# Performance work log

Measured on AMD Instinct MI355X. Metric: run time of the kernel, lower is better.

## Reference

```python
import jax, jax.numpy as jnp
import numpy as np

D_MODEL = 256; N_LAYERS = 4; INPUT_LEN = 15
D_INNER = 512; D_STATE = 16; D_CONV = 4; DT_RANK = 16
BATCH = 4; SEQ = 2048; EPS = 1e-5

def _ln(x, w, b):
    m = jnp.mean(x, -1, keepdims=True)
    v = jnp.var(x, -1, keepdims=True)
    return (x - m) * jax.lax.rsqrt(v + EPS) * w + b

def _silu(x):
    return x * jax.nn.sigmoid(x)

def _mixer(h, inW, cw, cb, xpW, dtW, dtb, A_log, Dp, opW):
    # h: [B,L,d_model]
    xz = h @ inW.T                      # [B,L,2*D_INNER]
    xh, z = jnp.split(xz, 2, axis=-1)
    # causal depthwise conv1d
    xc = jnp.transpose(xh, (0, 2, 1))   # [B,D,L]
    xc = jax.lax.conv_general_dilated(xc, cw, (1,), [(D_CONV - 1, 0)],
                                      feature_group_count=D_INNER,
                                      dimension_numbers=('NCH', 'OIH', 'NCH'))
    xc = xc + cb[None, :, None]
    xh = _silu(jnp.transpose(xc, (0, 2, 1)))  # [B,L,D]
    dbl = xh @ xpW.T                    # [B,L,DT_RANK+2N]
    dt = dbl[..., :DT_RANK]
    Bm = dbl[..., DT_RANK:DT_RANK + D_STATE]
    C = dbl[..., DT_RANK + D_STATE:]
    dt = jax.nn.softplus(dt @ dtW.T + dtb)    # [B,L,D]
    A = -jnp.exp(A_log)                       # [D,N]
    dA = jnp.exp(dt[..., None] * A)           # [B,L,D,N]
    dBu = dt[..., None] * Bm[:, :, None, :] * xh[..., None]  # [B,L,D,N]
    def step(hst, inp):
        dA_t, dBu_t, C_t = inp
        hst = dA_t * hst + dBu_t
        y = jnp.einsum('bdn,bn->bd', hst, C_t)
        return hst, y
    h0 = jnp.zeros((xh.shape[0], D_INNER, D_STATE), xh.dtype)
    _, ys = jax.lax.scan(step, h0, (jnp.transpose(dA, (1, 0, 2, 3)),
                                    jnp.transpose(dBu, (1, 0, 2, 3)),
                                    jnp.transpose(C, (1, 0, 2))))
    y = jnp.transpose(ys, (1, 0, 2)) + Dp * xh
    y = y * _silu(z)
    return y @ opW.T

def setup_inputs():
    key = jax.random.key(0)
    ks = jax.random.split(key, 8)
    s = 0.02
    return {
        'x_src': jax.random.normal(ks[0], (BATCH, SEQ, INPUT_LEN), jnp.float32),
        'single_eval_pos': 1024,
        'in_W': jax.random.normal(ks[1], (D_MODEL, INPUT_LEN)) * s,
        'norm_w': jnp.ones((N_LAYERS, D_MODEL)),
        'norm_b': jnp.zeros((N_LAYERS, D_MODEL)),
        'inproj_W': jax.random.normal(ks[2], (N_LAYERS, 2 * D_INNER, D_MODEL)) * s,
        'conv_w': jax.random.normal(ks[3], (N_LAYERS, D_INNER, 1, D_CONV)) * 0.2,
        'conv_b': jnp.zeros((N_LAYERS, D_INNER)),
        'xproj_W': jax.random.normal(ks[4], (N_LAYERS, DT_RANK + 2 * D_STATE, D_INNER)) * s,
        'dtproj_W': jax.random.normal(ks[5], (N_LAYERS, D_INNER, DT_RANK)) * 0.1,
        'dtproj_b': jnp.log(jnp.expm1(jnp.full((N_LAYERS, D_INNER), 0.01))),
        'A_log': jnp.log(jnp.broadcast_to(jnp.arange(1, D_STATE + 1, dtype=jnp.float32), (N_LAYERS, D_INNER, D_STATE)) + 0.0),
        'D_param': jnp.ones((N_LAYERS, D_INNER)),
        'outproj_W': jax.random.normal(ks[6], (N_LAYERS, D_MODEL, D_INNER)) * s,
        'out_W': jax.random.normal(ks[7], (1, D_MODEL)) * s,
    }

def reference(x_src, single_eval_pos, in_W, norm_w, norm_b, inproj_W, conv_w, conv_b, xproj_W, dtproj_W, dtproj_b, A_log, D_param, outproj_W, out_W):
    h = x_src @ in_W.T                  # [B,L,d_model]
    res = None
    for i in range(N_LAYERS):
        res = h if res is None else h + res
        hn = _ln(res, norm_w[i], norm_b[i])
        h = _mixer(hn, inproj_W[i], conv_w[i], conv_b[i], xproj_W[i],
                   dtproj_W[i], dtproj_b[i], A_log[i], D_param[i], outproj_W[i])
    # backbone returns hidden_states directly (norm_f defined but not applied)
    return h @ out_W.T                  # [B,L,1]
```

## Files before the change

kernel.cpp:

```cpp
#include <hip/hip_runtime.h>

#define B_   4
#define T_   2048
#define BT_  8192
#define INL  15
#define DM   256
#define DI   512
#define DX   1024
#define DS_  16
#define DR_  16
#define NO_  48
#define NL   4
#define NC_  128
#define LCH  16

typedef short bf16x8 __attribute__((ext_vector_type(8)));
typedef float f32x4  __attribute__((ext_vector_type(4)));

__device__ __forceinline__ float sigmoidf_(float x){ return 1.f/(1.f+__expf(-x)); }

__device__ __forceinline__ unsigned short f2bf(float x){
    union { float f; unsigned u; } v; v.f = x;
    unsigned r = (v.u + 0x7FFFu + ((v.u >> 16) & 1u)) >> 16;
    return (unsigned short)r;
}
__device__ __forceinline__ float bf2f(unsigned short h){
    union { unsigned u; float f; } v; v.u = ((unsigned)h) << 16;
    return v.f;
}

__device__ __forceinline__ void ld16(const float* __restrict__ p, float* v){
    const float4* q = (const float4*)p;
    float4 x0=q[0],x1=q[1],x2=q[2],x3=q[3];
    v[0]=x0.x; v[1]=x0.y; v[2]=x0.z; v[3]=x0.w;
    v[4]=x1.x; v[5]=x1.y; v[6]=x1.z; v[7]=x1.w;
    v[8]=x2.x; v[9]=x2.y; v[10]=x2.z; v[11]=x2.w;
    v[12]=x3.x; v[13]=x3.y; v[14]=x3.z; v[15]=x3.w;
}
__device__ __forceinline__ void st16(float* __restrict__ p, const float* v){
    float4* q = (float4*)p;
    q[0] = make_float4(v[0],v[1],v[2],v[3]);
    q[1] = make_float4(v[4],v[5],v[6],v[7]);
    q[2] = make_float4(v[8],v[9],v[10],v[11]);
    q[3] = make_float4(v[12],v[13],v[14],v[15]);
}

__global__ void k_cvtW3(const float* __restrict__ W0, unsigned short* __restrict__ h0,
                        unsigned short* __restrict__ l0, int n0,
                        const float* __restrict__ W1, unsigned short* __restrict__ h1,
                        unsigned short* __restrict__ l1, int n1,
                        const float* __restrict__ W2, unsigned short* __restrict__ h2,
                        unsigned short* __restrict__ l2, int n2){
    int g = blockIdx.x*256 + threadIdx.x;
    const float* W; unsigned short *hi, *lo; int idx;
    if(g < n0){ W = W0; hi = h0; lo = l0; idx = g; }
    else if(g < n0+n1){ W = W1; hi = h1; lo = l1; idx = g - n0; }
    else if(g < n0+n1+n2){ W = W2; hi = h2; lo = l2; idx = g - n0 - n1; }
    else return;
    float4 v = ((const float4*)W)[idx];
    ushort4 h, l;
    h.x = f2bf(v.x); l.x = f2bf(v.x - bf2f(h.x));
    h.y = f2bf(v.y); l.y = f2bf(v.y - bf2f(h.y));
    h.z = f2bf(v.z); l.z = f2bf(v.z - bf2f(h.z));
    h.w = f2bf(v.w); l.w = f2bf(v.w - bf2f(h.w));
    ((ushort4*)hi)[idx] = h;
    ((ushort4*)lo)[idx] = l;
}

__global__ void k_inln(const float* __restrict__ x, const float* __restrict__ W,
                       float* __restrict__ res,
                       unsigned short* __restrict__ hnhi, unsigned short* __restrict__ hnlo,
                       const float* __restrict__ w, const float* __restrict__ b){
    int wv = threadIdx.x >> 6, lane = threadIdx.x & 63;
    int bt = blockIdx.x*4 + wv;
    const float* xr = x + bt*INL;
    float xl[INL];
#pragma unroll
    for(int k=0;k<INL;k++) xl[k] = xr[k];
    float4 v;
    float* vv = (float*)&v;
#pragma unroll
    for(int j=0;j<4;j++){
        int m = lane*4 + j;
        const float* wr = W + m*INL;
        float acc = 0.f;
#pragma unroll
        for(int k=0;k<INL;k++) acc += xl[k]*wr[k];
        vv[j] = acc;
    }
    ((float4*)(res + (size_t)bt*DM))[lane] = v;
    float s  = v.x+v.y+v.z+v.w;
    float ss = v.x*v.x+v.y*v.y+v.z*v.z+v.w*v.w;
#pragma unroll
    for(int m=1;m<64;m<<=1){ s += __shfl_xor(s,m); ss += __shfl_xor(ss,m); }
    float mean = s*(1.f/DM);
    float var  = ss*(1.f/DM) - mean*mean;
    float inv  = rsqrtf(var + 1e-5f);
    float4 wt = ((const float4*)w)[lane];
    float4 bs = ((const float4*)b)[lane];
    float4 o;
    o.x = (v.x-mean)*inv*wt.x + bs.x;
    o.y = (v.y-mean)*inv*wt.y + bs.y;
    o.z = (v.z-mean)*inv*wt.z + bs.z;
    o.w = (v.w-mean)*inv*wt.w + bs.w;
    ushort4 hh, ll;
    hh.x = f2bf(o.x); ll.x = f2bf(o.x - bf2f(hh.x));
    hh.y = f2bf(o.y); ll.y = f2bf(o.y - bf2f(hh.y));
    hh.z = f2bf(o.z); ll.z = f2bf(o.z - bf2f(hh.z));
    hh.w = f2bf(o.w); ll.w = f2bf(o.w - bf2f(hh.w));
    ((ushort4*)(hnhi + (size_t)bt*DM))[lane] = hh;
    ((ushort4*)(hnlo + (size_t)bt*DM))[lane] = ll;
}

__global__ void k_resln(const float* __restrict__ h, float* __restrict__ res,
                        unsigned short* __restrict__ hnhi, unsigned short* __restrict__ hnlo,
                        const float* __restrict__ w, const float* __restrict__ b, int addRes){
    int wv = threadIdx.x >> 6, lane = threadIdx.x & 63;
    int bt = blockIdx.x*4 + wv;
    float4 v = ((const float4*)(h + (size_t)bt*DM))[lane];
    if(addRes){
        float4 r = ((const float4*)(res + (size_t)bt*DM))[lane];
        v.x+=r.x; v.y+=r.y; v.z+=r.z; v.w+=r.w;
    }
    ((float4*)(res + (size_t)bt*DM))[lane] = v;
    float s  = v.x+v.y+v.z+v.w;
    float ss = v.x*v.x+v.y*v.y+v.z*v.z+v.w*v.w;
#pragma unroll
    for(int m=1;m<64;m<<=1){ s += __shfl_xor(s,m); ss += __shfl_xor(ss,m); }
    float mean = s*(1.f/DM);
    float var  = ss*(1.f/DM) - mean*mean;
    float inv  = rsqrtf(var + 1e-5f);
    float4 wt = ((const float4*)w)[lane];
    float4 bs = ((const float4*)b)[lane];
    float4 o;
    o.x = (v.x-mean)*inv*wt.x + bs.x;
    o.y = (v.y-mean)*inv*wt.y + bs.y;
    o.z = (v.z-mean)*inv*wt.z + bs.z;
    o.w = (v.w-mean)*inv*wt.w + bs.w;
    ushort4 hh, ll;
    hh.x = f2bf(o.x); ll.x = f2bf(o.x - bf2f(hh.x));
    hh.y = f2bf(o.y); ll.y = f2bf(o.y - bf2f(hh.y));
    hh.z = f2bf(o.z); ll.z = f2bf(o.z - bf2f(hh.z));
    hh.w = f2bf(o.w); ll.w = f2bf(o.w - bf2f(hh.w));
    ((ushort4*)(hnhi + (size_t)bt*DM))[lane] = hh;
    ((ushort4*)(hnlo + (size_t)bt*DM))[lane] = ll;
}

template<int BM,int BN>
__global__ void __launch_bounds__(256) k_gemm_bf3(
    const unsigned short* __restrict__ Ahi, const unsigned short* __restrict__ Alo,
    const unsigned short* __restrict__ Bhi, const unsigned short* __restrict__ Blo,
    float* __restrict__ C, int M, int N, int K)
{
    constexpr int LDP = 40;
    constexpr int WM = BM/2, WN = BN/2;
    constexpr int MI_ = WM/16, NI_ = WN/16;
    __shared__ unsigned short sAh[BM*LDP], sAl[BM*LDP], sBh[BN*LDP], sBl[BN*LDP];
    int tid  = threadIdx.x;
    int wave = tid >> 6, lane = tid & 63;
    int wm0  = (wave >> 1) * WM, wn0 = (wave & 1) * WN;
    int m0   = blockIdx.y * BM, n0 = blockIdx.x * BN;
    int lr   = lane & 15;
    int kq   = (lane >> 4) * 8;
    int quad4 = (lane >> 4) * 4;

    f32x4 acc[MI_][NI_];
#pragma unroll
    for(int i=0;i<MI_;i++)
#pragma unroll
        for(int j=0;j<NI_;j++) acc[i][j] = (f32x4){0.f,0.f,0.f,0.f};

    for(int k0=0;k0<K;k0+=32){
#pragma unroll
        for(int i=tid;i<BM*4;i+=256){
            int r = i>>2, cg = (i&3)*8;
            size_t go = (size_t)(m0+r)*K + k0 + cg;
            *(float4*)(&sAh[r*LDP + cg]) = *(const float4*)(Ahi + go);
            *(float4*)(&sAl[r*LDP + cg]) = *(const float4*)(Alo + go);
        }
#pragma unroll
        for(int i=tid;i<BN*4;i+=256){
            int r = i>>2, cg = (i&3)*8;
            size_t go = (size_t)(n0+r)*K + k0 + cg;
            *(float4*)(&sBh[r*LDP + cg]) = *(const float4*)(Bhi + go);
            *(float4*)(&sBl[r*LDP + cg]) = *(const float4*)(Blo + go);
        }
        __syncthreads();
        bf16x8 ah[MI_], al[MI_], bh[NI_], bl[NI_];
#pragma unroll
        for(int mi=0;mi<MI_;mi++){
            int ro = (wm0 + mi*16 + lr)*LDP + kq;
            ah[mi] = *(const bf16x8*)(&sAh[ro]);
            al[mi] = *(const bf16x8*)(&sAl[ro]);
        }
#pragma unroll
        for(int ni=0;ni<NI_;ni++){
            int ro = (wn0 + ni*16 + lr)*LDP + kq;
            bh[ni] = *(const bf16x8*)(&sBh[ro]);
            bl[ni] = *(const bf16x8*)(&sBl[ro]);
        }
#pragma unroll
        for(int mi=0;mi<MI_;mi++)
#pragma unroll
            for(int ni=0;ni<NI_;ni++){
                acc[mi][ni] = __builtin_amdgcn_mfma_f32_16x16x32_bf16(ah[mi], bh[ni], acc[mi][ni], 0,0,0);
                acc[mi][ni] = __builtin_amdgcn_mfma_f32_16x16x32_bf16(ah[mi], bl[ni], acc[mi][ni], 0,0,0);
                acc[mi][ni] = __builtin_amdgcn_mfma_f32_16x16x32_bf16(al[mi], bh[ni], acc[mi][ni], 0,0,0);
            }
        __syncthreads();
    }
#pragma unroll
    for(int mi=0;mi<MI_;mi++)
#pragma unroll
        for(int ni=0;ni<NI_;ni++){
            int col = n0 + wn0 + ni*16 + lr;
#pragma unroll
            for(int r=0;r<4;r++){
                int row = m0 + wm0 + mi*16 + quad4 + r;
                C[(size_t)row*N + col] = acc[mi][ni][r];
            }
        }
}

template<int BM,int BN>
__global__ void __launch_bounds__(256) k_gemm_pk(
    const unsigned* __restrict__ Apk,
    const unsigned short* __restrict__ Bhi, const unsigned short* __restrict__ Blo,
    float* __restrict__ C, int M, int N, int K)
{
    constexpr int LDP = 40;
    constexpr int WM = BM/2, WN = BN/2;
    constexpr int MI_ = WM/16, NI_ = WN/16;
    __shared__ unsigned short sAh[BM*LDP], sAl[BM*LDP], sBh[BN*LDP], sBl[BN*LDP];
    int tid  = threadIdx.x;
    int wave = tid >> 6, lane = tid & 63;
    int wm0  = (wave >> 1) * WM, wn0 = (wave & 1) * WN;
    int m0   = blockIdx.y * BM, n0 = blockIdx.x * BN;
    int lr   = lane & 15;
    int kq   = (lane >> 4) * 8;
    int quad4 = (lane >> 4) * 4;

    f32x4 acc[MI_][NI_];
#pragma unroll
    for(int i=0;i<MI_;i++)
#pragma unroll
        for(int j=0;j<NI_;j++) acc[i][j] = (f32x4){0.f,0.f,0.f,0.f};

    for(int k0=0;k0<K;k0+=32){
#pragma unroll
        for(int i=tid;i<BM*2;i+=256){
            int r = i>>1, hf = (i&1)*16;
            const uint4* yp = (const uint4*)(Apk + (size_t)(m0+r)*K + k0 + hf);
#pragma unroll
            for(int q=0;q<4;q++){
                uint4 p = yp[q];
                ushort4 H, L;
                H.x=(unsigned short)p.x;  L.x=(unsigned short)(p.x>>16);
                H.y=(unsigned short)p.y;  L.y=(unsigned short)(p.y>>16);
                H.z=(unsigned short)p.z;  L.z=(unsigned short)(p.z>>16);
                H.w=(unsigned short)p.w;  L.w=(unsigned short)(p.w>>16);
                *(ushort4*)(&sAh[r*LDP + hf + q*4]) = H;
                *(ushort4*)(&sAl[r*LDP + hf + q*4]) = L;
            }
        }
#pragma unroll
        for(int i=tid;i<BN*4;i+=256){
            int r = i>>2, cg = (i&3)*8;
            size_t go = (size_t)(n0+r)*K + k0 + cg;
            *(float4*)(&sBh[r*LDP + cg]) = *(const float4*)(Bhi + go);
            *(float4*)(&sBl[r*LDP + cg]) = *(const float4*)(Blo + go);
        }
        __syncthreads();
        bf16x8 ah[MI_], al[MI_], bh[NI_], bl[NI_];
#pragma unroll
        for(int mi=0;mi<MI_;mi++){
            int ro = (wm0 + mi*16 + lr)*LDP + kq;
            ah[mi] = *(const bf16x8*)(&sAh[ro]);
            al[mi] = *(const bf16x8*)(&sAl[ro]);
        }
#pragma unroll
        for(int ni=0;ni<NI_;ni++){
            int ro = (wn0 + ni*16 + lr)*LDP + kq;
            bh[ni] = *(const bf16x8*)(&sBh[ro]);
            bl[ni] = *(const bf16x8*)(&sBl[ro]);
        }
#pragma unroll
        for(int mi=0;mi<MI_;mi++)
#pragma unroll
            for(int ni=0;ni<NI_;ni++){
                acc[mi][ni] = __builtin_amdgcn_mfma_f32_16x16x32_bf16(ah[mi], bh[ni], acc[mi][ni], 0,0,0);
                acc[mi][ni] = __builtin_amdgcn_mfma_f32_16x16x32_bf16(ah[mi], bl[ni], acc[mi][ni], 0,0,0);
                acc[mi][ni] = __builtin_amdgcn_mfma_f32_16x16x32_bf16(al[mi], bh[ni], acc[mi][ni], 0,0,0);
            }
        __syncthreads();
    }
#pragma unroll
    for(int mi=0;mi<MI_;mi++)
#pragma unroll
        for(int ni=0;ni<NI_;ni++){
            int col = n0 + wn0 + ni*16 + lr;
#pragma unroll
            for(int r=0;r<4;r++){
                int row = m0 + wm0 + mi*16 + quad4 + r;
                C[(size_t)row*N + col] = acc[mi][ni][r];
            }
        }
}

__global__ void __launch_bounds__(512) k_convxp2(
    const float* __restrict__ xz, const float* __restrict__ cw, const float* __restrict__ cb,
    const unsigned short* __restrict__ Bhi, const unsigned short* __restrict__ Blo,
    const float* __restrict__ dtW, const float* __restrict__ dtbias,
    float* __restrict__ xh, float* __restrict__ bc, float* __restrict__ dtO)
{
    __shared__ unsigned short sAh[16*520], sAl[16*520];
    __shared__ float dls[16*17];

    int tid = threadIdx.x;
    int wave = tid >> 6, lane = tid & 63;
    int lr = lane & 15, kq = (lane>>4)*8, quad4 = (lane>>4)*4;
    int m0 = blockIdx.x * LCH;
    int d  = tid;

    float xv[19];
    {
        int rbase = m0 - 3;
        bool mask0 = ((m0 & (T_-1)) == 0);
#pragma unroll
        for(int j=0;j<19;j++)
            xv[j] = (mask0 && j<3) ? 0.f : xz[(size_t)(rbase+j)*DX + d];
    }
    float4 w4 = *(const float4*)(cw + d*4);
    float bias = cb[d];
#pragma unroll
    for(int t=0;t<16;t++){
        float a = bias + w4.x*xv[t] + w4.y*xv[t+1] + w4.z*xv[t+2] + w4.w*xv[t+3];
        float v = a * sigmoidf_(a);
        xh[(size_t)(m0+t)*DI + d] = v;
        unsigned short hh = f2bf(v);
        sAh[t*520 + d] = hh;
        sAl[t*520 + d] = f2bf(v - bf2f(hh));
    }
    float wr_[16]; ld16(dtW + (size_t)d*16, wr_);
    float bsv = dtbias[d];
    __syncthreads();

    f32x4 acc = {0.f,0.f,0.f,0.f};
    if(wave < 3){
#pragma unroll 4
        for(int ks=0;ks<16;ks++){
            int ao = lr*520 + ks*32 + kq;
            bf16x8 ah = *(const bf16x8*)(&sAh[ao]);
            bf16x8 al = *(const bf16x8*)(&sAl[ao]);
            size_t wo = (size_t)(wave*16 + lr)*DI + ks*32 + kq;
            bf16x8 bh = *(const bf16x8*)(Bhi + wo);
            bf16x8 bl = *(const bf16x8*)(Blo + wo);
            acc = __builtin_amdgcn_mfma_f32_16x16x32_bf16(ah, bh, acc, 0,0,0);
            acc = __builtin_amdgcn_mfma_f32_16x16x32_bf16(ah, bl, acc, 0,0,0);
            acc = __builtin_amdgcn_mfma_f32_16x16x32_bf16(al, bh, acc, 0,0,0);
        }
        if(wave == 0){
#pragma unroll
            for(int r=0;r<4;r++) dls[(quad4+r)*17 + lr] = acc[r];
        } else if(wave == 1){
#pragma unroll
            for(int r=0;r<4;r++) bc[(size_t)(m0+quad4+r)*32 + lr] = acc[r];
        } else {
#pragma unroll
            for(int r=0;r<4;r++) bc[(size_t)(m0+quad4+r)*32 + 16 + lr] = acc[r];
        }
    }
    __syncthreads();

#pragma unroll
    for(int t=0;t<16;t++){
        float acc2 = bsv;
#pragma unroll
        for(int r=0;r<16;r++) acc2 += dls[t*17 + r]*wr_[r];
        float sp = fmaxf(acc2,0.f) + log1pf(__expf(-fabsf(acc2)));
        dtO[(size_t)(m0+t)*DI + d] = sp;
    }
}

__global__ void __launch_bounds__(256) k_scan1(const float* __restrict__ dt,
    const float* __restrict__ xh, const float* __restrict__ bc,
    const float* __restrict__ A_log, float* __restrict__ S, float* __restrict__ sdt){
    int d = blockIdx.x*256 + threadIdx.x;
    int c = blockIdx.y, b = blockIdx.z;
    float a_[16]; ld16(A_log + (size_t)d*16, a_);
#pragma unroll
    for(int n=0;n<16;n++) a_[n] = -__expf(a_[n]);
    float st_[16];
#pragma unroll
    for(int n=0;n<16;n++) st_[n] = 0.f;
    float sd = 0.f;
    int base = b*T_ + c*LCH;
#pragma unroll 4
    for(int t=0;t<LCH;t++){
        int bt = base + t;
        float dtv = dt[(size_t)bt*DI + d];
        float xhv = xh[(size_t)bt*DI + d];
        float bv[16]; ld16(bc + (size_t)bt*32, bv);
        float dx = dtv*xhv;
        sd += dtv;
#pragma unroll
        for(int n=0;n<16;n++) st_[n] = __expf(dtv*a_[n])*st_[n] + dx*bv[n];
    }
    st16(S + (((size_t)b*NC_ + c)*DI + d)*16, st_);
    sdt[((size_t)b*NC_ + c)*DI + d] = sd;
}

__global__ void k_scan2(const float* __restrict__ S, const float* __restrict__ sdt,
                        const float* __restrict__ A_log, float* __restrict__ Hinit){
    int g = blockIdx.x*256 + threadIdx.x;
    int b = g >> 13;
    int dn = g & 8191;
    int d = dn >> 4;
    float a = -__expf(A_log[dn]);
    float H = 0.f;
    for(int c=0;c<NC_;c++){
        size_t o = ((size_t)(b*NC_ + c))*8192 + dn;
        Hinit[o] = H;
        float sd = sdt[(size_t)(b*NC_ + c)*DI + d];
        H = __expf(sd*a)*H + S[o];
    }
}

__global__ void __launch_bounds__(256) k_scan3(
    const float* __restrict__ dt, const float* __restrict__ xh, const float* __restrict__ xz,
    const float* __restrict__ bc, const float* __restrict__ A_log, const float* __restrict__ Dpar,
    const float* __restrict__ Hinit, unsigned* __restrict__ Y)
{
    __shared__ float sbc[16*36];
    int tid = threadIdx.x;
    int c = blockIdx.y, b = blockIdx.z;
    int m0 = b*T_ + c*LCH;
    if(tid < 128){
        int t = tid >> 3, s = tid & 7;
        *(float4*)(&sbc[t*36 + s*4]) = *(const float4*)(bc + (size_t)(m0+t)*32 + s*4);
    }
    __syncthreads();
    int d = blockIdx.x*256 + tid;
    float a_[16]; ld16(A_log + (size_t)d*16, a_);
#pragma unroll
    for(int n=0;n<16;n++) a_[n] = -__expf(a_[n]);
    float st_[16]; ld16(Hinit + (((size_t)b*NC_ + c)*DI + d)*16, st_);
    float Dp = Dpar[d];
#pragma unroll 4
    for(int t=0;t<LCH;t++){
        int bt = m0 + t;
        float dtv = dt[(size_t)bt*DI + d];
        float xhv = xh[(size_t)bt*DI + d];
        float bv[16]; ld16(&sbc[t*36], bv);
        float cv[16]; ld16(&sbc[t*36 + 16], cv);
        float dx = dtv*xhv;
        float y = 0.f;
#pragma unroll
        for(int n=0;n<16;n++){
            st_[n] = __expf(dtv*a_[n])*st_[n] + dx*bv[n];
            y += st_[n]*cv[n];
        }
        float zv = xz[(size_t)bt*DX + DI + d];
        y += Dp*xhv;
        y = y * zv * sigmoidf_(zv);
        unsigned short hh = f2bf(y);
        unsigned short ll = f2bf(y - bf2f(hh));
        Y[(size_t)bt*DI + d] = (unsigned)hh | ((unsigned)ll << 16);
    }
}

__global__ void k_outw(const float* __restrict__ h, const float* __restrict__ ow,
                       float* __restrict__ out){
    int wv = threadIdx.x >> 6, lane = threadIdx.x & 63;
    int bt = blockIdx.x*4 + wv;
    float4 v = ((const float4*)(h + (size_t)bt*DM))[lane];
    float4 w = ((const float4*)ow)[lane];
    float s = v.x*w.x + v.y*w.y + v.z*w.z + v.w*w.w;
#pragma unroll
    for(int m=1;m<64;m<<=1) s += __shfl_xor(s,m);
    if(lane==0) out[bt] = s;
}

extern "C" void kernel_launch(void* const* d_in, const int* in_sizes, int n_in,
                              void* d_out, int out_size, void* d_ws, size_t ws_size,
                              hipStream_t stream){
    const float* x_src    = (const float*)d_in[0];
    const float* in_W     = (const float*)d_in[2];
    const float* norm_w   = (const float*)d_in[3];
    const float* norm_b   = (const float*)d_in[4];
    const float* inproj_W = (const float*)d_in[5];
    const float* conv_w   = (const float*)d_in[6];
    const float* conv_b   = (const float*)d_in[7];
    const float* xproj_W  = (const float*)d_in[8];
    const float* dtproj_W = (const float*)d_in[9];
    const float* dtproj_b = (const float*)d_in[10];
    const float* A_log    = (const float*)d_in[11];
    const float* D_param  = (const float*)d_in[12];
    const float* outproj_W= (const float*)d_in[13];
    const float* out_W    = (const float*)d_in[14];

    float* ws  = (float*)d_ws;
    float* h    = ws;
    float* res  = h    + (size_t)BT_*DM;
    float* xz   = res  + (size_t)BT_*DM;
    float* xh   = xz   + (size_t)BT_*DX;
    float* bcb  = xh   + (size_t)BT_*DI;
    float* dtb  = bcb  + (size_t)BT_*32;
    float* sdtb = dtb  + (size_t)BT_*DI;
    float* Sbuf = sdtb + (size_t)B_*NC_*DI;
    float* Hbuf = Sbuf + (size_t)B_*NC_*DI*DS_;
    unsigned short* us = (unsigned short*)(Hbuf + (size_t)B_*NC_*DI*DS_);
    unsigned short* WhiIn  = us;
    unsigned short* WloIn  = WhiIn  + (size_t)NL*DX*DM;
    unsigned short* WhiOut = WloIn  + (size_t)NL*DX*DM;
    unsigned short* WloOut = WhiOut + (size_t)NL*DM*DI;
    unsigned short* WhiXp  = WloOut + (size_t)NL*DM*DI;
    unsigned short* WloXp  = WhiXp  + (size_t)NL*NO_*DI;
    unsigned short* hnhi   = WloXp  + (size_t)NL*NO_*DI;
    unsigned short* hnlo   = hnhi   + (size_t)BT_*DM;
    unsigned*       ybuf   = (unsigned*)(hnlo + (size_t)BT_*DM);

    int n0 = NL*DX*DM/4, n1 = NL*DM*DI/4, n2 = NL*NO_*DI/4;
    k_cvtW3<<<(n0+n1+n2 + 255)/256, 256, 0, stream>>>(
        inproj_W,  WhiIn,  WloIn,  n0,
        outproj_W, WhiOut, WloOut, n1,
        xproj_W,   WhiXp,  WloXp,  n2);
    k_inln<<<BT_/4, 256, 0, stream>>>(x_src, in_W, res, hnhi, hnlo, norm_w, norm_b);
    for(int i=0;i<NL;i++){
        if(i > 0)
            k_resln<<<BT_/4, 256, 0, stream>>>(h, res, hnhi, hnlo, norm_w + i*DM, norm_b + i*DM, 1);
        k_gemm_bf3<128,128><<<dim3(DX/128, BT_/128), 256, 0, stream>>>(
            hnhi, hnlo, WhiIn + (size_t)i*DX*DM, WloIn + (size_t)i*DX*DM, xz, BT_, DX, DM);
        k_convxp2<<<BT_/LCH, 512, 0, stream>>>(xz, conv_w + i*DI*4, conv_b + i*DI,
            WhiXp + (size_t)i*NO_*DI, WloXp + (size_t)i*NO_*DI,
            dtproj_W + (size_t)i*DI*DR_, dtproj_b + i*DI, xh, bcb, dtb);
        k_scan1<<<dim3(2, NC_, B_), 256, 0, stream>>>(dtb, xh, bcb,
            A_log + (size_t)i*DI*DS_, Sbuf, sdtb);
        k_scan2<<<B_*DI*DS_/256, 256, 0, stream>>>(Sbuf, sdtb, A_log + (size_t)i*DI*DS_, Hbuf);
        k_scan3<<<dim3(2, NC_, B_), 256, 0, stream>>>(dtb, xh, xz, bcb, A_log + (size_t)i*DI*DS_,
            D_param + i*DI, Hbuf, ybuf);
        k_gemm_pk<128,64><<<dim3(DM/64, BT_/128), 256, 0, stream>>>(
            ybuf, WhiOut + (size_t)i*DM*DI, WloOut + (size_t)i*DM*DI, h, BT_, DM, DI);
    }
    k_outw<<<BT_/4, 256, 0, stream>>>(h, out_W, (float*)d_out);
}
```

Baseline: 614.2 us.

## Recompute dt projection in scan kernels instead of materializing dt buffer

The dt projection and softplus move out of the conv/xproj kernel, which now writes only the 48-wide dbl rows. Each scan kernel recomputes dt from those rows plus the dtproj weights, so the BT×DI dt buffer is no longer written and read twice per layer. The x_proj MFMA is also split across 6 waves with K halves, its B-weights prefetched into registers before the conv loop, and the partial sums reduced through shared memory. The cost is duplicated dt math in scan1 and scan3, more register pressure, and faster reciprocal and log intrinsics that change rounding slightly.

```diff
diff --git a/kernel.cpp b/kernel.cpp
--- a/kernel.cpp
+++ b/kernel.cpp
@@ -17,7 +17,12 @@
 typedef short bf16x8 __attribute__((ext_vector_type(8)));
 typedef float f32x4  __attribute__((ext_vector_type(4)));
 
-__device__ __forceinline__ float sigmoidf_(float x){ return 1.f/(1.f+__expf(-x)); }
+__device__ __forceinline__ float sigmoidf_(float x){
+    return __builtin_amdgcn_rcpf(1.f + __expf(-x));
+}
+__device__ __forceinline__ float softplusf_(float x){
+    return fmaxf(x, 0.f) + __logf(1.f + __expf(-fabsf(x)));
+}
 
 __device__ __forceinline__ unsigned short f2bf(float x){
     union { float f; unsigned u; } v; v.f = x;
@@ -310,17 +315,17 @@
 __global__ void __launch_bounds__(512) k_convxp2(
     const float* __restrict__ xz, const float* __restrict__ cw, const float* __restrict__ cb,
     const unsigned short* __restrict__ Bhi, const unsigned short* __restrict__ Blo,
-    const float* __restrict__ dtW, const float* __restrict__ dtbias,
-    float* __restrict__ xh, float* __restrict__ bc, float* __restrict__ dtO)
+    float* __restrict__ xh, float* __restrict__ dbl)
 {
     __shared__ unsigned short sAh[16*520], sAl[16*520];
-    __shared__ float dls[16*17];
+    __shared__ float sP[6][16][20];
 
     int tid = threadIdx.x;
     int wave = tid >> 6, lane = tid & 63;
     int lr = lane & 15, kq = (lane>>4)*8, quad4 = (lane>>4)*4;
     int m0 = blockIdx.x * LCH;
     int d  = tid;
+    int nt = wave >> 1, kh = wave & 1;
 
     float xv[19];
     {
@@ -329,6 +334,16 @@
 #pragma unroll
         for(int j=0;j<19;j++)
             xv[j] = (mask0 && j<3) ? 0.f : xz[(size_t)(rbase+j)*DX + d];
+    }
+    bf16x8 pbh[8], pbl[8];
+    if(wave < 6){
+        const unsigned short* bhp = Bhi + (size_t)(nt*16 + lr)*DI + kh*256 + kq;
+        const unsigned short* blp = Blo + (size_t)(nt*16 + lr)*DI + kh*256 + kq;
+#pragma unroll
+        for(int ks=0;ks<8;ks++){
+            pbh[ks] = *(const bf16x8*)(bhp + ks*32);
+            pbl[ks] = *(const bf16x8*)(blp + ks*32);
+        }
     }
     float4 w4 = *(const float4*)(cw + d*4);
     float bias = cb[d];
@@ -341,55 +356,44 @@
         sAh[t*520 + d] = hh;
         sAl[t*520 + d] = f2bf(v - bf2f(hh));
     }
-    float wr_[16]; ld16(dtW + (size_t)d*16, wr_);
-    float bsv = dtbias[d];
     __syncthreads();
 
-    f32x4 acc = {0.f,0.f,0.f,0.f};
-    if(wave < 3){
-#pragma unroll 4
-        for(int ks=0;ks<16;ks++){
-            int ao = lr*520 + ks*32 + kq;
+    if(wave < 6){
+        f32x4 acc = {0.f,0.f,0.f,0.f};
+#pragma unroll
+        for(int ks=0;ks<8;ks++){
+            int ao = lr*520 + kh*256 + ks*32 + kq;
             bf16x8 ah = *(const bf16x8*)(&sAh[ao]);
             bf16x8 al = *(const bf16x8*)(&sAl[ao]);
-            size_t wo = (size_t)(wave*16 + lr)*DI + ks*32 + kq;
-            bf16x8 bh = *(const bf16x8*)(Bhi + wo);
-            bf16x8 bl = *(const bf16x8*)(Blo + wo);
-            acc = __builtin_amdgcn_mfma_f32_16x16x32_bf16(ah, bh, acc, 0,0,0);
-            acc = __builtin_amdgcn_mfma_f32_16x16x32_bf16(ah, bl, acc, 0,0,0);
-            acc = __builtin_amdgcn_mfma_f32_16x16x32_bf16(al, bh, acc, 0,0,0);
-        }
-        if(wave == 0){
-#pragma unroll
-            for(int r=0;r<4;r++) dls[(quad4+r)*17 + lr] = acc[r];
-        } else if(wave == 1){
-#pragma unroll
-            for(int r=0;r<4;r++) bc[(size_t)(m0+quad4+r)*32 + lr] = acc[r];
-        } else {
-#pragma unroll
-            for(int r=0;r<4;r++) bc[(size_t)(m0+quad4+r)*32 + 16 + lr] = acc[r];
-        }
+            acc = __builtin_amdgcn_mfma_f32_16x16x32_bf16(ah, pbh[ks], acc, 0,0,0);
+            acc = __builtin_amdgcn_mfma_f32_16x16x32_bf16(ah, pbl[ks], acc, 0,0,0);
+            acc = __builtin_amdgcn_mfma_f32_16x16x32_bf16(al, pbh[ks], acc, 0,0,0);
+        }
+#pragma unroll
+        for(int r=0;r<4;r++) sP[wave][quad4+r][lr] = acc[r];
     }
     __syncthreads();
 
-#pragma unroll
-    for(int t=0;t<16;t++){
-        float acc2 = bsv;
-#pragma unroll
-        for(int r=0;r<16;r++) acc2 += dls[t*17 + r]*wr_[r];
-        float sp = fmaxf(acc2,0.f) + log1pf(__expf(-fabsf(acc2)));
-        dtO[(size_t)(m0+t)*DI + d] = sp;
-    }
-}
-
-__global__ void __launch_bounds__(256) k_scan1(const float* __restrict__ dt,
-    const float* __restrict__ xh, const float* __restrict__ bc,
-    const float* __restrict__ A_log, float* __restrict__ S, float* __restrict__ sdt){
+    for(int i=tid;i<768;i+=512){
+        int t = i/48, n = i - t*48;
+        int nt2 = n >> 4, nn = n & 15;
+        float v = sP[nt2*2][t][nn] + sP[nt2*2+1][t][nn];
+        dbl[(size_t)(m0+t)*48 + n] = v;
+    }
+}
+
+__global__ void __launch_bounds__(256) k_scan1(
+    const float* __restrict__ dbl, const float* __restrict__ xh,
+    const float* __restrict__ dtW, const float* __restrict__ dtbias,
+    const float* __restrict__ A_log, float* __restrict__ S, float* __restrict__ sdt)
+{
     int d = blockIdx.x*256 + threadIdx.x;
     int c = blockIdx.y, b = blockIdx.z;
     float a_[16]; ld16(A_log + (size_t)d*16, a_);
 #pragma unroll
     for(int n=0;n<16;n++) a_[n] = -__expf(a_[n]);
+    float wr_[16]; ld16(dtW + (size_t)d*16, wr_);
+    float bsv = dtbias[d];
     float st_[16];
 #pragma unroll
     for(int n=0;n<16;n++) st_[n] = 0.f;
@@ -398,9 +402,13 @@
 #pragma unroll 4
     for(int t=0;t<LCH;t++){
         int bt = base + t;
-        float dtv = dt[(size_t)bt*DI + d];
+        float dl[16]; ld16(dbl + (size_t)bt*48, dl);
+        float bv[16]; ld16(dbl + (size_t)bt*48 + 16, bv);
+        float pre = bsv;
+#pragma unroll
+        for(int r=0;r<16;r++) pre += dl[r]*wr_[r];
+        float dtv = softplusf_(pre);
         float xhv = xh[(size_t)bt*DI + d];
-        float bv[16]; ld16(bc + (size_t)bt*32, bv);
         float dx = dtv*xhv;
         sd += dtv;
 #pragma unroll
@@ -427,32 +435,39 @@
 }
 
 __global__ void __launch_bounds__(256) k_scan3(
-    const float* __restrict__ dt, const float* __restrict__ xh, const float* __restrict__ xz,
-    const float* __restrict__ bc, const float* __restrict__ A_log, const float* __restrict__ Dpar,
+    const float* __restrict__ dbl, const float* __restrict__ xh, const float* __restrict__ xz,
+    const float* __restrict__ A_log, const float* __restrict__ Dpar,
+    const float* __restrict__ dtW, const float* __restrict__ dtbias,
     const float* __restrict__ Hinit, unsigned* __restrict__ Y)
 {
-    __shared__ float sbc[16*36];
+    __shared__ float sbc[16*52];
     int tid = threadIdx.x;
     int c = blockIdx.y, b = blockIdx.z;
     int m0 = b*T_ + c*LCH;
-    if(tid < 128){
-        int t = tid >> 3, s = tid & 7;
-        *(float4*)(&sbc[t*36 + s*4]) = *(const float4*)(bc + (size_t)(m0+t)*32 + s*4);
+    if(tid < 192){
+        int t = tid/12, s = tid - t*12;
+        *(float4*)(&sbc[t*52 + s*4]) = *(const float4*)(dbl + (size_t)(m0+t)*48 + s*4);
     }
     __syncthreads();
     int d = blockIdx.x*256 + tid;
     float a_[16]; ld16(A_log + (size_t)d*16, a_);
 #pragma unroll
     for(int n=0;n<16;n++) a_[n] = -__expf(a_[n]);
+    float wr_[16]; ld16(dtW + (size_t)d*16, wr_);
+    float bsv = dtbias[d];
     float st_[16]; ld16(Hinit + (((size_t)b*NC_ + c)*DI + d)*16, st_);
     float Dp = Dpar[d];
-#pragma unroll 4
+#pragma unroll 2
     for(int t=0;t<LCH;t++){
         int bt = m0 + t;
-        float dtv = dt[(size_t)bt*DI + d];
+        float dl[16]; ld16(&sbc[t*52], dl);
+        float bv[16]; ld16(&sbc[t*52 + 16], bv);
+        float cv[16]; ld16(&sbc[t*52 + 32], cv);
+        float pre = bsv;
+#pragma unroll
+        for(int r=0;r<16;r++) pre += dl[r]*wr_[r];
+        float dtv = softplusf_(pre);
         float xhv = xh[(size_t)bt*DI + d];
-        float bv[16]; ld16(&sbc[t*36], bv);
-        float cv[16]; ld16(&sbc[t*36 + 16], cv);
         float dx = dtv*xhv;
         float y = 0.f;
 #pragma unroll
@@ -504,9 +519,8 @@
     float* res  = h    + (size_t)BT_*DM;
     float* xz   = res  + (size_t)BT_*DM;
     float* xh   = xz   + (size_t)BT_*DX;
-    float* bcb  = xh   + (size_t)BT_*DI;
-    float* dtb  = bcb  + (size_t)BT_*32;
-    float* sdtb = dtb  + (size_t)BT_*DI;
+    float* dbl  = xh   + (size_t)BT_*DI;
+    float* sdtb = dbl  + (size_t)BT_*48;
     float* Sbuf = sdtb + (size_t)B_*NC_*DI;
     float* Hbuf = Sbuf + (size_t)B_*NC_*DI*DS_;
     unsigned short* us = (unsigned short*)(Hbuf + (size_t)B_*NC_*DI*DS_);
@@ -532,13 +546,14 @@
         k_gemm_bf3<128,128><<<dim3(DX/128, BT_/128), 256, 0, stream>>>(
             hnhi, hnlo, WhiIn + (size_t)i*DX*DM, WloIn + (size_t)i*DX*DM, xz, BT_, DX, DM);
         k_convxp2<<<BT_/LCH, 512, 0, stream>>>(xz, conv_w + i*DI*4, conv_b + i*DI,
-            WhiXp + (size_t)i*NO_*DI, WloXp + (size_t)i*NO_*DI,
-            dtproj_W + (size_t)i*DI*DR_, dtproj_b + i*DI, xh, bcb, dtb);
-        k_scan1<<<dim3(2, NC_, B_), 256, 0, stream>>>(dtb, xh, bcb,
+            WhiXp + (size_t)i*NO_*DI, WloXp + (size_t)i*NO_*DI, xh, dbl);
+        k_scan1<<<dim3(2, NC_, B_), 256, 0, stream>>>(dbl, xh,
+            dtproj_W + (size_t)i*DI*DR_, dtproj_b + i*DI,
             A_log + (size_t)i*DI*DS_, Sbuf, sdtb);
         k_scan2<<<B_*DI*DS_/256, 256, 0, stream>>>(Sbuf, sdtb, A_log + (size_t)i*DI*DS_, Hbuf);
-        k_scan3<<<dim3(2, NC_, B_), 256, 0, stream>>>(dtb, xh, xz, bcb, A_log + (size_t)i*DI*DS_,
-            D_param + i*DI, Hbuf, ybuf);
+        k_scan3<<<dim3(2, NC_, B_), 256, 0, stream>>>(dbl, xh, xz,
+            A_log + (size_t)i*DI*DS_, D_param + i*DI,
+            dtproj_W + (size_t)i*DI*DR_, dtproj_b + i*DI, Hbuf, ybuf);
         k_gemm_pk<128,64><<<dim3(DM/64, BT_/128), 256, 0, stream>>>(
             ybuf, WhiOut + (size_t)i*DM*DI, WloOut + (size_t)i*DM*DI, h, BT_, DM, DI);
     }
```

New measurement: 579.1 us. 5.7% less time.
